# Optimization experiments

Hardware: AMD Instinct MI355X
Metric: run time of the kernel (lower is better)

## Reference

```python
import jax, jax.numpy as jnp
import numpy as np

N_NODES = 100000
N_EDGES = 3200000
IN_DIM = 128
HIDDEN = 128
N_GRAPHS = 64


def setup_inputs() -> dict:
    key = jax.random.key(0)
    ks = jax.random.split(key, 16)
    feat = jax.random.normal(ks[0], (N_NODES, IN_DIM), dtype=jnp.float32)
    src = jax.random.randint(ks[1], (N_EDGES,), 0, N_NODES, dtype=jnp.int32)
    dst = jax.random.randint(ks[2], (N_EDGES,), 0, N_NODES, dtype=jnp.int32)
    graph_ids = jnp.sort(jax.random.randint(ks[3], (N_NODES,), 0, N_GRAPHS, dtype=jnp.int32))
    # GraphConv weights (in_feats, out_feats) + bias, DGL default glorot-ish scale
    def lin(k, fi, fo):
        s = 1.0 / np.sqrt(fi)
        kw, kb = jax.random.split(k)
        W = jax.random.uniform(kw, (fi, fo), jnp.float32, -s, s)
        b = jax.random.uniform(kb, (fo,), jnp.float32, -s, s)
        return W, b
    W1, b1 = lin(ks[4], IN_DIM, HIDDEN)
    W2, b2 = lin(ks[5], HIDDEN, HIDDEN)
    # MLPReadout(128, 1, L=3): 128->64->32->16->1
    Wm0, bm0 = lin(ks[6], 128, 64)
    Wm1, bm1 = lin(ks[7], 64, 32)
    Wm2, bm2 = lin(ks[8], 32, 16)
    Wm3, bm3 = lin(ks[9], 16, 1)
    return dict(feat=feat, src=src, dst=dst, graph_ids=graph_ids, num_graphs=N_GRAPHS,
                W1=W1, b1=b1, W2=W2, b2=b2,
                Wm0=Wm0, bm0=bm0, Wm1=Wm1, bm1=bm1, Wm2=Wm2, bm2=bm2, Wm3=Wm3, bm3=bm3)


def reference(feat, src, dst, graph_ids, num_graphs,
              W1, b1, W2, b2,
              Wm0, bm0, Wm1, bm1, Wm2, bm2, Wm3, bm3):
    N = feat.shape[0]
    ones_e = jnp.ones(src.shape[0], dtype=feat.dtype)
    # DGL GraphConv norm='both': D_out^{-1/2} on src side, D_in^{-1/2} on dst side,
    # degrees clamped to >=1 (allow_zero_in_degree=True)
    deg_out = jnp.clip(jax.ops.segment_sum(ones_e, src, num_segments=N), 1.0)
    deg_in = jnp.clip(jax.ops.segment_sum(ones_e, dst, num_segments=N), 1.0)
    norm_src = jax.lax.rsqrt(deg_out)[:, None]  # [N,1]
    norm_dst = jax.lax.rsqrt(deg_in)[:, None]

    def gconv(h, W, b):
        h = h * norm_src
        agg = jax.ops.segment_sum(h[src], dst, num_segments=N)  # SpMM: [N,d]
        return agg * norm_dst @ W + b

    h = jax.nn.relu(gconv(feat, W1, b1))
    h = jax.nn.relu(gconv(h, W2, b2))

    # dgl.mean_nodes: per-graph mean over nodes
    counts = jnp.clip(jax.ops.segment_sum(jnp.ones(N, dtype=h.dtype), graph_ids, num_segments=num_graphs), 1.0)
    hg = jax.ops.segment_sum(h, graph_ids, num_segments=num_graphs) / counts[:, None]  # [G, hidden]

    # MLPReadout
    y = jax.nn.relu(hg @ Wm0 + bm0)
    y = jax.nn.relu(y @ Wm1 + bm1)
    y = jax.nn.relu(y @ Wm2 + bm2)
    return y @ Wm3 + bm3  # [G, 1]
```

## Files before the change

kernel.cpp:

```cpp
#include <hip/hip_runtime.h>
#include <hip/hip_fp16.h>

#define N_NODES 100000
#define N_EDGES 3200000
#define DIM 128
#define NG 64
#define GS_CHUNKS 16

#define KSH 9
#define BKT 512
#define NBKT ((N_NODES + BKT - 1) / BKT)
#define CHUNK 16384
#define NBLK ((N_EDGES + CHUNK - 1) / CHUNK)

using f16x8 = __attribute__((ext_vector_type(8))) _Float16;
using f32x4 = __attribute__((ext_vector_type(4))) float;

__global__ __launch_bounds__(256) void k_hist1(const int* __restrict__ src, const int* __restrict__ dst,
                                               int* __restrict__ histD, int* __restrict__ histS,
                                               int* __restrict__ rowtot) {
    __shared__ int hD[NBKT];
    __shared__ int hS[NBKT];
    int t = threadIdx.x, blk = blockIdx.x;
    for (int i = t; i < NBKT; i += 256) { hD[i] = 0; hS[i] = 0; }
    __syncthreads();
    int base = blk * CHUNK;
    for (int i = t; i < CHUNK; i += 256) {
        int e = base + i;
        if (e < N_EDGES) {
            atomicAdd(&hD[dst[e] >> KSH], 1);
            atomicAdd(&hS[src[e] >> KSH], 1);
        }
    }
    __syncthreads();
    for (int i = t; i < NBKT; i += 256) {
        histD[i * NBLK + blk] = hD[i];
        histS[i * NBLK + blk] = hS[i];
        atomicAdd(&rowtot[i], hD[i]);
        atomicAdd(&rowtot[NBKT + i], hS[i]);
    }
}

__global__ __launch_bounds__(256) void k_rowapply(int* __restrict__ histD, int* __restrict__ histS,
                                                  const int* __restrict__ rowtot) {
    __shared__ int sh[256];
    __shared__ int red[256];
    int r = blockIdx.x;
    int half = (r < NBKT) ? 0 : 1;
    int pos = half ? (r - NBKT) : r;
    int* a = half ? (histS + (size_t)pos * NBLK) : (histD + (size_t)pos * NBLK);
    int t = threadIdx.x;
    red[t] = (t < pos) ? rowtot[half * NBKT + t] : 0;
    __syncthreads();
    for (int off = 128; off > 0; off >>= 1) {
        if (t < off) red[t] += red[t + off];
        __syncthreads();
    }
    int basev = red[0];
    int x = (t < NBLK) ? a[t] : 0;
    sh[t] = x; __syncthreads();
    for (int off = 1; off < 256; off <<= 1) {
        int y = sh[t]; int u = (t >= off) ? sh[t - off] : 0;
        __syncthreads(); sh[t] = y + u; __syncthreads();
    }
    if (t < NBLK) a[t] = sh[t] - x + basev;
}

__global__ __launch_bounds__(256) void k_scatter1(const int* __restrict__ src, const int* __restrict__ dst,
                                                  const int* __restrict__ histD, const int* __restrict__ histS,
                                                  int* __restrict__ bufD, unsigned short* __restrict__ bufS) {
    __shared__ int cD[NBKT];
    __shared__ int cS[NBKT];
    int t = threadIdx.x, blk = blockIdx.x;
    for (int i = t; i < NBKT; i += 256) {
        cD[i] = histD[i * NBLK + blk];
        cS[i] = histS[i * NBLK + blk];
    }
    __syncthreads();
    int base = blk * CHUNK;
    for (int i = t; i < CHUNK; i += 256) {
        int e = base + i;
        if (e < N_EDGES) {
            int s = src[e], d = dst[e];
            int pD = atomicAdd(&cD[d >> KSH], 1);
            bufD[pD] = ((d & (BKT - 1)) << 17) | s;
            int pS = atomicAdd(&cS[s >> KSH], 1);
            bufS[pS] = (unsigned short)(s & (BKT - 1));
        }
    }
}

__global__ __launch_bounds__(256) void k_pass2s(const unsigned short* __restrict__ bufS,
                                                const int* __restrict__ histS,
                                                float* __restrict__ norm_src) {
    __shared__ int binc[BKT];
    int b = blockIdx.x, t = threadIdx.x;
    int start = histS[b * NBLK];
    int end = (b + 1 < NBKT) ? histS[(b + 1) * NBLK] : N_EDGES;
    for (int i = t; i < BKT; i += 256) binc[i] = 0;
    __syncthreads();
    for (int i = start + t; i < end; i += 256) atomicAdd(&binc[bufS[i]], 1);
    __syncthreads();
    int nb = N_NODES - b * BKT; if (nb > BKT) nb = BKT;
    for (int j = t; j < nb; j += 256) {
        int c = binc[j]; if (c < 1) c = 1;
        norm_src[b * BKT + j] = rsqrtf((float)c);
    }
}

__global__ __launch_bounds__(256) void k_pass2(const int* __restrict__ bufD,
                                               const int* __restrict__ histD,
                                               int* __restrict__ rowptr, float* __restrict__ norm_dst,
                                               int* __restrict__ col) {
    __shared__ int binc[BKT];
    __shared__ int binoff[BKT];
    int b = blockIdx.x, t = threadIdx.x;
    int start = histD[b * NBLK];
    int end = (b + 1 < NBKT) ? histD[(b + 1) * NBLK] : N_EDGES;
    for (int i = t; i < BKT; i += 256) binc[i] = 0;
    __syncthreads();
    for (int i = start + t; i < end; i += 256) atomicAdd(&binc[bufD[i] >> 17], 1);
    __syncthreads();
    if (t < 64) {
        int base8 = t * 8;
        int loc[8]; int s8 = 0;
        #pragma unroll
        for (int k = 0; k < 8; k++) { loc[k] = s8; s8 += binc[base8 + k]; }
        int x = s8;
        #pragma unroll
        for (int off = 1; off < 64; off <<= 1) {
            int y = __shfl_up(x, off);
            if (t >= off) x += y;
        }
        int excl = x - s8;
        #pragma unroll
        for (int k = 0; k < 8; k++) binoff[base8 + k] = excl + loc[k];
    }
    __syncthreads();
    int nb = N_NODES - b * BKT; if (nb > BKT) nb = BKT;
    for (int j = t; j < nb; j += 256) {
        rowptr[b * BKT + j] = start + binoff[j];
        int c = binc[j]; if (c < 1) c = 1;
        norm_dst[b * BKT + j] = rsqrtf((float)c);
    }
    if (b == NBKT - 1 && t == 0) rowptr[N_NODES] = N_EDGES;
    __syncthreads();
    for (int i = t; i < BKT; i += 256) binc[i] = binoff[i];
    __syncthreads();
    for (int i = start + t; i < end; i += 256) {
        int v = bufD[i];
        int ld = v >> 17, s = v & 0x1FFFF;
        int p = atomicAdd(&binc[ld], 1);
        col[start + p] = s;
    }
}

__global__ __launch_bounds__(256) void k_cast8(const float* __restrict__ in,
                                               const float* __restrict__ norm_src,
                                               unsigned* __restrict__ out) {
    int i4 = blockIdx.x * 256 + threadIdx.x;
    const int TOT = N_NODES * DIM / 4;
    if (i4 >= TOT) return;
    int row = i4 >> 5;
    float sc = norm_src[row];
    float4 v = ((const float4*)in)[i4];
    unsigned w = 0;
    w = __builtin_amdgcn_cvt_pk_fp8_f32(v.x * sc, v.y * sc, w, 0);
    w = __builtin_amdgcn_cvt_pk_fp8_f32(v.z * sc, v.w * sc, w, 1);
    out[i4] = w;
}

#define ACC8(r) do {                                                                  \
    auto p0 = __builtin_amdgcn_cvt_pk_f32_fp8((r).x, 0); a0 += p0[0]; a1 += p0[1];    \
    auto p1 = __builtin_amdgcn_cvt_pk_f32_fp8((r).x, 1); a2 += p1[0]; a3 += p1[1];    \
    auto p2 = __builtin_amdgcn_cvt_pk_f32_fp8((r).y, 0); a4 += p2[0]; a5 += p2[1];    \
    auto p3 = __builtin_amdgcn_cvt_pk_f32_fp8((r).y, 1); a6 += p3[0]; a7 += p3[1];    \
    auto p4 = __builtin_amdgcn_cvt_pk_f32_fp8((r).z, 0); a8 += p4[0]; a9 += p4[1];    \
    auto p5 = __builtin_amdgcn_cvt_pk_f32_fp8((r).z, 1); a10 += p5[0]; a11 += p5[1];  \
    auto p6 = __builtin_amdgcn_cvt_pk_f32_fp8((r).w, 0); a12 += p6[0]; a13 += p6[1];  \
    auto p7 = __builtin_amdgcn_cvt_pk_f32_fp8((r).w, 1); a14 += p7[0]; a15 += p7[1];  \
} while (0)

__global__ __launch_bounds__(256) void k_spmm8(const unsigned char* __restrict__ in,
                       const int* __restrict__ rowptr, const int* __restrict__ col,
                       const float* __restrict__ norm_dst, __half2* __restrict__ out) {
    int wid = (blockIdx.x * 256 + threadIdx.x) >> 6;
    int lane = threadIdx.x & 63;
    int rg = lane >> 3, l8 = lane & 7;
    int node = wid * 8 + rg;
    if (node >= N_NODES) return;
    int jb = rowptr[node], je = rowptr[node + 1];
    float a0 = 0.f, a1 = 0.f, a2 = 0.f, a3 = 0.f, a4 = 0.f, a5 = 0.f, a6 = 0.f, a7 = 0.f;
    float a8 = 0.f, a9 = 0.f, a10 = 0.f, a11 = 0.f, a12 = 0.f, a13 = 0.f, a14 = 0.f, a15 = 0.f;
    int j = jb;
    for (; j + 2 <= je; j += 2) {
        int s0 = col[j], s1 = col[j + 1];
        uint4 r0 = *(const uint4*)&in[(size_t)s0 * 128 + l8 * 16];
        uint4 r1 = *(const uint4*)&in[(size_t)s1 * 128 + l8 * 16];
        ACC8(r0);
        ACC8(r1);
    }
    if (j < je) {
        int s0 = col[j];
        uint4 r0 = *(const uint4*)&in[(size_t)s0 * 128 + l8 * 16];
        ACC8(r0);
    }
    float nd = norm_dst[node];
    __half2 h0 = __floats2half2_rn(a0 * nd, a1 * nd);
    __half2 h1 = __floats2half2_rn(a2 * nd, a3 * nd);
    __half2 h2 = __floats2half2_rn(a4 * nd, a5 * nd);
    __half2 h3 = __floats2half2_rn(a6 * nd, a7 * nd);
    __half2 h4 = __floats2half2_rn(a8 * nd, a9 * nd);
    __half2 h5 = __floats2half2_rn(a10 * nd, a11 * nd);
    __half2 h6 = __floats2half2_rn(a12 * nd, a13 * nd);
    __half2 h7 = __floats2half2_rn(a14 * nd, a15 * nd);
    uint4 o0, o1;
    o0.x = *(unsigned*)&h0; o0.y = *(unsigned*)&h1;
    o0.z = *(unsigned*)&h2; o0.w = *(unsigned*)&h3;
    o1.x = *(unsigned*)&h4; o1.y = *(unsigned*)&h5;
    o1.z = *(unsigned*)&h6; o1.w = *(unsigned*)&h7;
    *(uint4*)&out[(size_t)node * 64 + l8 * 8] = o0;
    *(uint4*)&out[(size_t)node * 64 + l8 * 8 + 4] = o1;
}

template <bool SCALE, bool OUT8>
__global__ __launch_bounds__(256) void k_gemm_mfma(const __half* __restrict__ A,
        const float* __restrict__ W, const float* __restrict__ bias,
        const float* __restrict__ rowscale, void* __restrict__ outp) {
    __shared__ _Float16 lds[128 * 136];
    int tid = threadIdx.x;
    for (int idx = tid * 4; idx < DIM * DIM; idx += 256 * 4) {
        int k = idx >> 7, n = idx & 127;
        float4 w = *(const float4*)&W[idx];
        lds[(n + 0) * 136 + k] = (_Float16)w.x;
        lds[(n + 1) * 136 + k] = (_Float16)w.y;
        lds[(n + 2) * 136 + k] = (_Float16)w.z;
        lds[(n + 3) * 136 + k] = (_Float16)w.w;
    }
    __syncthreads();
    int wv = tid >> 6, lane = tid & 63;
    int rbase = blockIdx.x * 64 + wv * 16;
    int l15 = lane & 15, kg = lane >> 4;
    int arow = rbase + l15; if (arow >= N_NODES) arow = N_NODES - 1;
    const _Float16* Af = (const _Float16*)A + (size_t)arow * DIM + kg * 8;
    f16x8 a0 = *(const f16x8*)(Af + 0);
    f16x8 a1 = *(const f16x8*)(Af + 32);
    f16x8 a2 = *(const f16x8*)(Af + 64);
    f16x8 a3 = *(const f16x8*)(Af + 96);
    f32x4 acc[8];
    #pragma unroll
    for (int nt = 0; nt < 8; nt++) acc[nt] = (f32x4){0.f, 0.f, 0.f, 0.f};
    #pragma unroll
    for (int nt = 0; nt < 8; nt++) {
        const _Float16* bb = &lds[(nt * 16 + l15) * 136 + kg * 8];
        f16x8 b0 = *(const f16x8*)(bb + 0);
        f16x8 b1 = *(const f16x8*)(bb + 32);
        f16x8 b2 = *(const f16x8*)(bb + 64);
        f16x8 b3 = *(const f16x8*)(bb + 96);
        acc[nt] = __builtin_amdgcn_mfma_f32_16x16x32_f16(a0, b0, acc[nt], 0, 0, 0);
        acc[nt] = __builtin_amdgcn_mfma_f32_16x16x32_f16(a1, b1, acc[nt], 0, 0, 0);
        acc[nt] = __builtin_amdgcn_mfma_f32_16x16x32_f16(a2, b2, acc[nt], 0, 0, 0);
        acc[nt] = __builtin_amdgcn_mfma_f32_16x16x32_f16(a3, b3, acc[nt], 0, 0, 0);
    }
    __syncthreads();
    float bsc[4];
    #pragma unroll
    for (int r = 0; r < 4; r++) {
        if (SCALE) {
            int row = rbase + kg * 4 + r; if (row >= N_NODES) row = N_NODES - 1;
            bsc[r] = rowscale[row];
        } else bsc[r] = 1.f;
    }
    #pragma unroll
    for (int nt = 0; nt < 8; nt++) {
        float bv = bias[nt * 16 + l15];
        #pragma unroll
        for (int r = 0; r < 4; r++) {
            float v = fmaxf(acc[nt][r] + bv, 0.f) * bsc[r];
            lds[(size_t)(wv * 16 + kg * 4 + r) * 136 + nt * 16 + l15] = (_Float16)v;
        }
    }
    __syncthreads();
    #pragma unroll
    for (int t = 0; t < 4; t++) {
        int lrow = wv * 16 + t * 4 + kg;
        int grow = rbase + t * 4 + kg;
        f16x8 v = *(const f16x8*)&lds[(size_t)lrow * 136 + l15 * 8];
        if (grow < N_NODES) {
            if (OUT8) {
                unsigned w0 = 0, w1 = 0;
                w0 = __builtin_amdgcn_cvt_pk_fp8_f32((float)v[0], (float)v[1], w0, 0);
                w0 = __builtin_amdgcn_cvt_pk_fp8_f32((float)v[2], (float)v[3], w0, 1);
                w1 = __builtin_amdgcn_cvt_pk_fp8_f32((float)v[4], (float)v[5], w1, 0);
                w1 = __builtin_amdgcn_cvt_pk_fp8_f32((float)v[6], (float)v[7], w1, 1);
                uint2 o; o.x = w0; o.y = w1;
                *(uint2*)&((unsigned char*)outp)[(size_t)grow * 128 + l15 * 8] = o;
            } else {
                *(f16x8*)&((_Float16*)outp)[(size_t)grow * DIM + l15 * 8] = v;
            }
        }
    }
}

__global__ __launch_bounds__(256) void k_graphsum_part(const __half2* __restrict__ h,
                           const int* __restrict__ gids, float* __restrict__ partial) {
    __shared__ float redx[256];
    __shared__ float redy[256];
    __shared__ int sb[2];
    int g = blockIdx.x;
    int c = blockIdx.y;
    if (threadIdx.x == 0) {
        int lo = 0, hi = N_NODES;
        while (lo < hi) { int mid = (lo + hi) >> 1; if (gids[mid] < g) lo = mid + 1; else hi = mid; }
        sb[0] = lo;
        lo = 0; hi = N_NODES;
        while (lo < hi) { int mid = (lo + hi) >> 1; if (gids[mid] <= g) lo = mid + 1; else hi = mid; }
        sb[1] = lo;
    }
    __syncthreads();
    int s = sb[0], e = sb[1];
    int p = threadIdx.x & 63;
    int r = threadIdx.x >> 6;
    int clen = (e - s + GS_CHUNKS - 1) / GS_CHUNKS;
    int b0 = s + c * clen;
    int b1 = b0 + clen; if (b1 > e) b1 = e;
    float ax = 0.f, ay = 0.f;
    for (int nd = b0 + r; nd < b1; nd += 4) {
        float2 f = __half22float2(h[(size_t)nd * 64 + p]);
        ax += f.x; ay += f.y;
    }
    redx[threadIdx.x] = ax; redy[threadIdx.x] = ay;
    __syncthreads();
    if (threadIdx.x < 64) {
        float sx = redx[threadIdx.x] + redx[threadIdx.x + 64] + redx[threadIdx.x + 128] + redx[threadIdx.x + 192];
        float sy = redy[threadIdx.x] + redy[threadIdx.x + 64] + redy[threadIdx.x + 128] + redy[threadIdx.x + 192];
        float* pp = &partial[((size_t)g * GS_CHUNKS + c) * DIM];
        pp[2 * threadIdx.x] = sx;
        pp[2 * threadIdx.x + 1] = sy;
    }
}

__global__ __launch_bounds__(128) void k_mlp(const float* __restrict__ partial,
                      const int* __restrict__ gids,
                      const float* __restrict__ Wm0, const float* __restrict__ bm0,
                      const float* __restrict__ Wm1, const float* __restrict__ bm1,
                      const float* __restrict__ Wm2, const float* __restrict__ bm2,
                      const float* __restrict__ Wm3, const float* __restrict__ bm3,
                      float* __restrict__ out) {
    __shared__ float hb[DIM];
    __shared__ float l0[64];
    __shared__ float l1[32];
    __shared__ float l2[16];
    __shared__ int scnt;
    int g = blockIdx.x;
    int t = threadIdx.x;
    if (t == 0) {
        int lo = 0, hi = N_NODES;
        while (lo < hi) { int mid = (lo + hi) >> 1; if (gids[mid] < g) lo = mid + 1; else hi = mid; }
        int s = lo;
        lo = 0; hi = N_NODES;
        while (lo < hi) { int mid = (lo + hi) >> 1; if (gids[mid] <= g) lo = mid + 1; else hi = mid; }
        int c = lo - s; if (c < 1) c = 1;
        scnt = c;
    }
    __syncthreads();
    float acc = 0.f;
    #pragma unroll
    for (int c = 0; c < GS_CHUNKS; c++)
        acc += partial[((size_t)g * GS_CHUNKS + c) * DIM + t];
    hb[t] = acc / (float)scnt;
    __syncthreads();
    if (t < 64) {
        float a = bm0[t];
        for (int k = 0; k < 128; k++) a += hb[k] * Wm0[k * 64 + t];
        l0[t] = fmaxf(a, 0.f);
    }
    __syncthreads();
    if (t < 32) {
        float a = bm1[t];
        for (int k = 0; k < 64; k++) a += l0[k] * Wm1[k * 32 + t];
        l1[t] = fmaxf(a, 0.f);
    }
    __syncthreads();
    if (t < 16) {
        float a = bm2[t];
        for (int k = 0; k < 32; k++) a += l1[k] * Wm2[k * 16 + t];
        l2[t] = fmaxf(a, 0.f);
    }
    __syncthreads();
    if (t == 0) {
        float a = bm3[0];
        for (int k = 0; k < 16; k++) a += l2[k] * Wm3[k];
        out[g] = a;
    }
}

extern "C" void kernel_launch(void* const* d_in, const int* in_sizes, int n_in,
                              void* d_out, int out_size, void* d_ws, size_t ws_size,
                              hipStream_t stream) {
    const float* feat = (const float*)d_in[0];
    const int*   src  = (const int*)d_in[1];
    const int*   dst  = (const int*)d_in[2];
    const int*   gids = (const int*)d_in[3];
    const float* W1   = (const float*)d_in[5];
    const float* b1   = (const float*)d_in[6];
    const float* W2   = (const float*)d_in[7];
    const float* b2   = (const float*)d_in[8];
    const float* Wm0  = (const float*)d_in[9];
    const float* bm0  = (const float*)d_in[10];
    const float* Wm1  = (const float*)d_in[11];
    const float* bm1  = (const float*)d_in[12];
    const float* Wm2  = (const float*)d_in[13];
    const float* bm2  = (const float*)d_in[14];
    const float* Wm3  = (const float*)d_in[15];
    const float* bm3  = (const float*)d_in[16];
    float* out = (float*)d_out;

    char* ws = (char*)d_ws;
    size_t off = 0;
    auto alloc = [&](size_t bytes) -> void* {
        void* p = ws + off;
        off += (bytes + 511) & ~(size_t)511;
        return p;
    };
    float* norm_src = (float*)alloc((size_t)N_NODES * 4);
    float* norm_dst = (float*)alloc((size_t)N_NODES * 4);
    int* rowptr   = (int*)alloc((size_t)(N_NODES + 1) * 4);
    int* histD    = (int*)alloc((size_t)NBKT * NBLK * 4);
    int* histS    = (int*)alloc((size_t)NBKT * NBLK * 4);
    int* rowtot   = (int*)alloc((size_t)(2 * NBKT) * 4);
    int* bufD     = (int*)alloc((size_t)N_EDGES * 4);
    int* colbuf   = (int*)alloc((size_t)N_EDGES * 4);
    unsigned char* feat8 = (unsigned char*)alloc((size_t)N_NODES * DIM);
    unsigned char* h8    = (unsigned char*)alloc((size_t)N_NODES * DIM);
    __half* s16   = (__half*)alloc((size_t)N_NODES * DIM * 2);
    __half* g16   = (__half*)alloc((size_t)N_NODES * DIM * 2);
    float* partial = (float*)alloc((size_t)NG * GS_CHUNKS * DIM * 4);
    unsigned short* bufS = (unsigned short*)colbuf;
    int* col = colbuf;

    hipMemsetAsync(rowtot, 0, (size_t)(2 * NBKT) * 4, stream);

    k_hist1<<<NBLK, 256, 0, stream>>>(src, dst, histD, histS, rowtot);
    k_rowapply<<<2 * NBKT, 256, 0, stream>>>(histD, histS, rowtot);
    k_scatter1<<<NBLK, 256, 0, stream>>>(src, dst, histD, histS, bufD, bufS);
    k_pass2s<<<NBKT, 256, 0, stream>>>(bufS, histS, norm_src);
    k_pass2<<<NBKT, 256, 0, stream>>>(bufD, histD, rowptr, norm_dst, col);

    k_cast8<<<(N_NODES * DIM / 4 + 255) / 256, 256, 0, stream>>>(feat, norm_src, (unsigned*)feat8);

    int sb2 = (N_NODES + 31) / 32;
    int gb = (N_NODES + 63) / 64;
    k_spmm8<<<sb2, 256, 0, stream>>>(feat8, rowptr, col, norm_dst, (__half2*)s16);
    k_gemm_mfma<true, true><<<gb, 256, 0, stream>>>(s16, W1, b1, norm_src, h8);
    k_spmm8<<<sb2, 256, 0, stream>>>(h8, rowptr, col, norm_dst, (__half2*)s16);
    k_gemm_mfma<false, false><<<gb, 256, 0, stream>>>(s16, W2, b2, nullptr, g16);

    dim3 gsg(NG, GS_CHUNKS);
    k_graphsum_part<<<gsg, 256, 0, stream>>>((const __half2*)g16, gids, partial);
    k_mlp<<<NG, 128, 0, stream>>>(partial, gids, Wm0, bm0, Wm1, bm1, Wm2, bm2, Wm3, bm3, out);
}
```

Measured before the change: 369.7 us.

## Compute source out-degrees with global atomics instead of a bucket sort pass

Replaces the two-level bucket sort for source degrees (shared histogram, scatter to bufS, per-bucket counting kernel) with direct global atomicAdd into a per-node degS array during the histogram pass. The norm_src rsqrt is now computed inside the cast kernel, which also writes norm_src. This removes one kernel, the bufS scatter traffic and half of the rowapply work. In exchange it adds 3.2M global atomics on random addresses spread over 100K counters, plus an extra memset.

```diff
diff --git a/kernel.cpp b/kernel.cpp
--- a/kernel.cpp
+++ b/kernel.cpp
@@ -17,40 +17,35 @@
 using f32x4 = __attribute__((ext_vector_type(4))) float;
 
 __global__ __launch_bounds__(256) void k_hist1(const int* __restrict__ src, const int* __restrict__ dst,
-                                               int* __restrict__ histD, int* __restrict__ histS,
-                                               int* __restrict__ rowtot) {
+                                               int* __restrict__ histD, int* __restrict__ rowtot,
+                                               int* __restrict__ degS) {
     __shared__ int hD[NBKT];
-    __shared__ int hS[NBKT];
     int t = threadIdx.x, blk = blockIdx.x;
-    for (int i = t; i < NBKT; i += 256) { hD[i] = 0; hS[i] = 0; }
+    for (int i = t; i < NBKT; i += 256) hD[i] = 0;
     __syncthreads();
     int base = blk * CHUNK;
     for (int i = t; i < CHUNK; i += 256) {
         int e = base + i;
         if (e < N_EDGES) {
             atomicAdd(&hD[dst[e] >> KSH], 1);
-            atomicAdd(&hS[src[e] >> KSH], 1);
+            atomicAdd(&degS[src[e]], 1);
         }
     }
     __syncthreads();
     for (int i = t; i < NBKT; i += 256) {
         histD[i * NBLK + blk] = hD[i];
-        histS[i * NBLK + blk] = hS[i];
         atomicAdd(&rowtot[i], hD[i]);
-        atomicAdd(&rowtot[NBKT + i], hS[i]);
-    }
-}
-
-__global__ __launch_bounds__(256) void k_rowapply(int* __restrict__ histD, int* __restrict__ histS,
+    }
+}
+
+__global__ __launch_bounds__(256) void k_rowapply(int* __restrict__ histD,
                                                   const int* __restrict__ rowtot) {
     __shared__ int sh[256];
     __shared__ int red[256];
     int r = blockIdx.x;
-    int half = (r < NBKT) ? 0 : 1;
-    int pos = half ? (r - NBKT) : r;
-    int* a = half ? (histS + (size_t)pos * NBLK) : (histD + (size_t)pos * NBLK);
+    int* a = histD + (size_t)r * NBLK;
     int t = threadIdx.x;
-    red[t] = (t < pos) ? rowtot[half * NBKT + t] : 0;
+    red[t] = (t < r) ? rowtot[t] : 0;
     __syncthreads();
     for (int off = 128; off > 0; off >>= 1) {
         if (t < off) red[t] += red[t + off];
@@ -67,15 +62,11 @@
 }
 
 __global__ __launch_bounds__(256) void k_scatter1(const int* __restrict__ src, const int* __restrict__ dst,
-                                                  const int* __restrict__ histD, const int* __restrict__ histS,
-                                                  int* __restrict__ bufD, unsigned short* __restrict__ bufS) {
+                                                  const int* __restrict__ histD,
+                                                  int* __restrict__ bufD) {
     __shared__ int cD[NBKT];
-    __shared__ int cS[NBKT];
     int t = threadIdx.x, blk = blockIdx.x;
-    for (int i = t; i < NBKT; i += 256) {
-        cD[i] = histD[i * NBLK + blk];
-        cS[i] = histS[i * NBLK + blk];
-    }
+    for (int i = t; i < NBKT; i += 256) cD[i] = histD[i * NBLK + blk];
     __syncthreads();
     int base = blk * CHUNK;
     for (int i = t; i < CHUNK; i += 256) {
@@ -84,27 +75,7 @@
             int s = src[e], d = dst[e];
             int pD = atomicAdd(&cD[d >> KSH], 1);
             bufD[pD] = ((d & (BKT - 1)) << 17) | s;
-            int pS = atomicAdd(&cS[s >> KSH], 1);
-            bufS[pS] = (unsigned short)(s & (BKT - 1));
         }
-    }
-}
-
-__global__ __launch_bounds__(256) void k_pass2s(const unsigned short* __restrict__ bufS,
-                                                const int* __restrict__ histS,
-                                                float* __restrict__ norm_src) {
-    __shared__ int binc[BKT];
-    int b = blockIdx.x, t = threadIdx.x;
-    int start = histS[b * NBLK];
-    int end = (b + 1 < NBKT) ? histS[(b + 1) * NBLK] : N_EDGES;
-    for (int i = t; i < BKT; i += 256) binc[i] = 0;
-    __syncthreads();
-    for (int i = start + t; i < end; i += 256) atomicAdd(&binc[bufS[i]], 1);
-    __syncthreads();
-    int nb = N_NODES - b * BKT; if (nb > BKT) nb = BKT;
-    for (int j = t; j < nb; j += 256) {
-        int c = binc[j]; if (c < 1) c = 1;
-        norm_src[b * BKT + j] = rsqrtf((float)c);
     }
 }
 
@@ -156,13 +127,16 @@
 }
 
 __global__ __launch_bounds__(256) void k_cast8(const float* __restrict__ in,
-                                               const float* __restrict__ norm_src,
+                                               const int* __restrict__ degS,
+                                               float* __restrict__ norm_src,
                                                unsigned* __restrict__ out) {
     int i4 = blockIdx.x * 256 + threadIdx.x;
     const int TOT = N_NODES * DIM / 4;
     if (i4 >= TOT) return;
     int row = i4 >> 5;
-    float sc = norm_src[row];
+    int c = degS[row]; if (c < 1) c = 1;
+    float sc = rsqrtf((float)c);
+    if ((i4 & 31) == 0) norm_src[row] = sc;
     float4 v = ((const float4*)in)[i4];
     unsigned w = 0;
     w = __builtin_amdgcn_cvt_pk_fp8_f32(v.x * sc, v.y * sc, w, 0);
@@ -425,29 +399,27 @@
     };
     float* norm_src = (float*)alloc((size_t)N_NODES * 4);
     float* norm_dst = (float*)alloc((size_t)N_NODES * 4);
+    int* degS     = (int*)alloc((size_t)N_NODES * 4);
     int* rowptr   = (int*)alloc((size_t)(N_NODES + 1) * 4);
     int* histD    = (int*)alloc((size_t)NBKT * NBLK * 4);
-    int* histS    = (int*)alloc((size_t)NBKT * NBLK * 4);
-    int* rowtot   = (int*)alloc((size_t)(2 * NBKT) * 4);
+    int* rowtot   = (int*)alloc((size_t)NBKT * 4);
     int* bufD     = (int*)alloc((size_t)N_EDGES * 4);
-    int* colbuf   = (int*)alloc((size_t)N_EDGES * 4);
+    int* col      = (int*)alloc((size_t)N_EDGES * 4);
     unsigned char* feat8 = (unsigned char*)alloc((size_t)N_NODES * DIM);
     unsigned char* h8    = (unsigned char*)alloc((size_t)N_NODES * DIM);
     __half* s16   = (__half*)alloc((size_t)N_NODES * DIM * 2);
     __half* g16   = (__half*)alloc((size_t)N_NODES * DIM * 2);
     float* partial = (float*)alloc((size_t)NG * GS_CHUNKS * DIM * 4);
-    unsigned short* bufS = (unsigned short*)colbuf;
-    int* col = colbuf;
-
-    hipMemsetAsync(rowtot, 0, (size_t)(2 * NBKT) * 4, stream);
-
-    k_hist1<<<NBLK, 256, 0, stream>>>(src, dst, histD, histS, rowtot);
-    k_rowapply<<<2 * NBKT, 256, 0, stream>>>(histD, histS, rowtot);
-    k_scatter1<<<NBLK, 256, 0, stream>>>(src, dst, histD, histS, bufD, bufS);
-    k_pass2s<<<NBKT, 256, 0, stream>>>(bufS, histS, norm_src);
+
+    hipMemsetAsync(rowtot, 0, (size_t)NBKT * 4, stream);
+    hipMemsetAsync(degS, 0, (size_t)N_NODES * 4, stream);
+
+    k_hist1<<<NBLK, 256, 0, stream>>>(src, dst, histD, rowtot, degS);
+    k_rowapply<<<NBKT, 256, 0, stream>>>(histD, rowtot);
+    k_scatter1<<<NBLK, 256, 0, stream>>>(src, dst, histD, bufD);
     k_pass2<<<NBKT, 256, 0, stream>>>(bufD, histD, rowptr, norm_dst, col);
 
-    k_cast8<<<(N_NODES * DIM / 4 + 255) / 256, 256, 0, stream>>>(feat, norm_src, (unsigned*)feat8);
+    k_cast8<<<(N_NODES * DIM / 4 + 255) / 256, 256, 0, stream>>>(feat, degS, norm_src, (unsigned*)feat8);
 
     int sb2 = (N_NODES + 31) / 32;
     int gb = (N_NODES + 63) / 64;
```

After: 441.6 us. 1.19x slower.
